# Kernel tuning notes

Measured on AMD Instinct MI355X. Metric: run time of the kernel, lower is better.

Reference implementation:

```python
import jax, jax.numpy as jnp
import numpy as np


def setup_inputs() -> dict:
    key = jax.random.key(0)
    kq, kk, kv = jax.random.split(key, 3)
    B, H, N, D = 2, 16, 2048, 128
    q = jax.random.normal(kq, (B, H, N, D), dtype=jnp.float32)
    k = jax.random.normal(kk, (B, H, N, D), dtype=jnp.float32)
    v = jax.random.normal(kv, (B, H, N, D), dtype=jnp.float32)
    return {"q": q, "k": k, "v": v, "num_sink": 4, "window_size": 1024}


def reference(q, k, v, num_sink, window_size):
    # Sink + sliding-window causal attention (single-device path of the SP wrapper).
    # Query i attends to key j iff j <= i AND (j < num_sink OR i - j < window_size).
    B, H, N, D = q.shape
    scale = 1.0 / np.sqrt(D).astype(np.float32)
    i = jnp.arange(N)[:, None]   # query positions
    j = jnp.arange(N)[None, :]   # key positions
    mask = (j <= i) & ((j < num_sink) | ((i - j) < window_size))  # [N, N]
    scores = jnp.einsum('bhid,bhjd->bhij', q, k) * scale          # [B,H,N,N]
    scores = jnp.where(mask, scores, jnp.finfo(scores.dtype).min)
    attn = jax.nn.softmax(scores, axis=-1)
    return jnp.einsum('bhij,bhjd->bhid', attn, v)
```

## Files before the change

kernel.cpp:

```cpp
#include <hip/hip_runtime.h>
#include <stdint.h>

#define NN 2048
#define DD 128
#define BHH 32
#define QT 64
#define KT 64
#define NQT (NN / QT)

typedef short v8s __attribute__((ext_vector_type(8)));
typedef short v4s __attribute__((ext_vector_type(4)));
typedef float v4f __attribute__((ext_vector_type(4)));

__device__ __forceinline__ unsigned short f2bf(float x) {
  unsigned u = __builtin_bit_cast(unsigned, x);
  u += 0x7fffu + ((u >> 16) & 1u);
  return (unsigned short)(u >> 16);
}

__device__ __forceinline__ v8s cvt8(const float* __restrict__ p) {
  v8s r;
#pragma unroll
  for (int j = 0; j < 8; j++) r[j] = (short)f2bf(p[j]);
  return r;
}

__global__ void prep(const float* __restrict__ K, const float* __restrict__ V,
                     unsigned short* __restrict__ Kb, unsigned short* __restrict__ Vt) {
  const int z = blockIdx.z;
  const int tid = threadIdx.x;
  if (z >= BHH) {
    const int bh = z - BHH;
    const int chunk = blockIdx.y * 32 + blockIdx.x;
    size_t base = (size_t)bh * NN * DD + (size_t)chunk * 4096 + (size_t)tid * 16;
#pragma unroll
    for (int h = 0; h < 2; h++)
      *(v8s*)(Kb + base + h * 8) = cvt8(K + base + h * 8);
    return;
  }
  __shared__ unsigned short t[64 * 68];
  const int bh = z;
  const int n0 = blockIdx.x * 64, d0 = blockIdx.y * 64;
  const float* src = V + ((size_t)bh * NN + n0) * DD + d0;
#pragma unroll
  for (int p = 0; p < 4; p++) {
    int r = p * 16 + (tid >> 4);
    int c = (tid & 15) * 4;
    v4f f = *(const v4f*)(src + (size_t)r * DD + c);
    v4s u;
#pragma unroll
    for (int j = 0; j < 4; j++) u[j] = (short)f2bf(f[j]);
    *(v4s*)(t + r * 68 + c) = u;
  }
  __syncthreads();
  unsigned short* dst = Vt + ((size_t)bh * DD + d0) * NN + n0;
#pragma unroll
  for (int p = 0; p < 2; p++) {
    int d = p * 32 + (tid >> 3);
    int nc = (tid & 7) * 8;
    v8s o;
#pragma unroll
    for (int j = 0; j < 8; j++) o[j] = (short)t[(nc + j) * 68 + d];
    *(v8s*)(dst + (size_t)d * NN + nc) = o;
  }
}

template <bool KBF, bool USE_VT>
__global__ __launch_bounds__(256, 4) void attn(
    const float* __restrict__ Q,
    const float* __restrict__ Kf, const unsigned short* __restrict__ Kb,
    const unsigned short* __restrict__ Vt, const float* __restrict__ Vf,
    const int* __restrict__ nsp, const int* __restrict__ wsp,
    float* __restrict__ O) {
  const int ns = nsp[0], win = wsp[0];
  const int j = blockIdx.x;
  const int bh = j & 31;
  const int jobid = j >> 5;
  int qis[2], njobs;
  if (jobid < 16) { njobs = 1; qis[0] = 31 - jobid; qis[1] = 0; }
  else { int p = jobid - 16; njobs = 2; qis[0] = 15 - p; qis[1] = p; }

  const int tid = threadIdx.x;
  const int w = tid >> 6;
  const int l = tid & 63;
  const int lo = l & 15, q4 = l >> 4;

  __shared__ __align__(16) unsigned short Kl[KT * DD];
  __shared__ __align__(16) unsigned short Vl[KT * DD];
  __shared__ __align__(16) unsigned short Pl[4 * 16 * KT];

  const float csc = 0.088388347648318447f * 1.4426950408889634f;
  unsigned short* Pw = Pl + w * 1024;
  const int rb = q4 * 4;

  for (int ji = 0; ji < njobs; ji++) {
    const int q0 = qis[ji] * QT;
    const int qrow0 = q0 + w * 16;

    v8s qf[4];
    {
      const float* qb = Q + ((size_t)bh * NN + qrow0 + lo) * DD + q4 * 8;
#pragma unroll
      for (int kc = 0; kc < 4; kc++) qf[kc] = cvt8(qb + kc * 32);
    }

    float lsum[4];
    v4f oa[8];
#pragma unroll
    for (int r = 0; r < 4; r++) lsum[r] = 0.f;
#pragma unroll
    for (int nc = 0; nc < 8; nc++) oa[nc] = (v4f){0.f, 0.f, 0.f, 0.f};

    const size_t koff0 = ((size_t)bh * NN + w * 16 + lo) * DD + q4 * 8;

    for (int kb = 0; kb < q0 + QT; kb += KT) {
      if ((kb >= ns) && (kb + KT - 1 < q0 - win + 1)) continue;

      v8s kst[4];
      {
        size_t g = koff0 + (size_t)kb * DD;
#pragma unroll
        for (int kc = 0; kc < 4; kc++)
          kst[kc] = KBF ? *(const v8s*)(Kb + g + kc * 32) : cvt8(Kf + g + kc * 32);
      }
      v8s vst[4];
      if (USE_VT) {
#pragma unroll
        for (int i = 0; i < 4; i++) {
          int f = w * 4 + i, kt = f >> 3, nc = f & 7;
          vst[i] = *(const v8s*)(Vt + ((size_t)bh * DD + nc * 16 + lo) * NN + kb +
                                 kt * 32 + q4 * 8);
        }
      }

      __syncthreads();
#pragma unroll
      for (int kc = 0; kc < 4; kc++)
        *(v8s*)(Kl + (w * 4 + kc) * 512 + l * 8) = kst[kc];
      if (USE_VT) {
#pragma unroll
        for (int i = 0; i < 4; i++)
          *(v8s*)(Vl + (w * 4 + i) * 512 + l * 8) = vst[i];
      }
      __syncthreads();

      v4f s[4];
#pragma unroll
      for (int ct = 0; ct < 4; ct++) {
        s[ct] = (v4f){0.f, 0.f, 0.f, 0.f};
#pragma unroll
        for (int kc = 0; kc < 4; kc++) {
          v8s kf = *(const v8s*)(Kl + (ct * 4 + kc) * 512 + l * 8);
          s[ct] = __builtin_amdgcn_mfma_f32_16x16x32_bf16(qf[kc], kf, s[ct], 0, 0, 0);
        }
      }
#pragma unroll
      for (int ct = 0; ct < 4; ct++) {
        int kj = kb + ct * 16 + lo;
#pragma unroll
        for (int r = 0; r < 4; r++) {
          int qi = qrow0 + rb + r;
          bool valid = (kj <= qi) && ((kj < ns) || (qi - kj < win));
          s[ct][r] = valid ? __builtin_amdgcn_exp2f(s[ct][r] * csc) : 0.f;
        }
      }
#pragma unroll
      for (int r = 0; r < 4; r++)
        lsum[r] += (s[0][r] + s[1][r]) + (s[2][r] + s[3][r]);

#pragma unroll
      for (int ct = 0; ct < 4; ct++) {
#pragma unroll
        for (int r = 0; r < 4; r++) {
          int row = rb + r;
          int idx = (ct >> 1) * 512 + (row + 16 * ((ct & 1) * 2 + ((l >> 3) & 1))) * 8 + (l & 7);
          Pw[idx] = f2bf(s[ct][r]);
        }
      }
#pragma unroll
      for (int kt = 0; kt < 2; kt++) {
        v8s pf = *(const v8s*)(Pw + kt * 512 + l * 8);
#pragma unroll
        for (int nc = 0; nc < 8; nc++) {
          v8s vf;
          if (USE_VT) {
            vf = *(const v8s*)(Vl + (kt * 8 + nc) * 512 + l * 8);
          } else {
#pragma unroll
            for (int jj = 0; jj < 8; jj++) {
              size_t vi = ((size_t)bh * NN + kb + kt * 32 + q4 * 8 + jj) * DD + nc * 16 + lo;
              vf[jj] = (short)f2bf(Vf[vi]);
            }
          }
          oa[nc] = __builtin_amdgcn_mfma_f32_16x16x32_bf16(pf, vf, oa[nc], 0, 0, 0);
        }
      }
    }

    float inv[4];
#pragma unroll
    for (int r = 0; r < 4; r++) {
      float v = lsum[r];
      v += __shfl_xor(v, 1, 64);
      v += __shfl_xor(v, 2, 64);
      v += __shfl_xor(v, 4, 64);
      v += __shfl_xor(v, 8, 64);
      inv[r] = 1.f / v;
    }
    float* ob = O + ((size_t)bh * NN + qrow0) * DD;
#pragma unroll
    for (int nc = 0; nc < 8; nc++)
#pragma unroll
      for (int r = 0; r < 4; r++)
        ob[(size_t)(rb + r) * DD + nc * 16 + lo] = oa[nc][r] * inv[r];
  }
}

extern "C" void kernel_launch(void* const* d_in, const int* in_sizes, int n_in,
                              void* d_out, int out_size, void* d_ws, size_t ws_size,
                              hipStream_t stream) {
  const float* q = (const float*)d_in[0];
  const float* k = (const float*)d_in[1];
  const float* v = (const float*)d_in[2];
  const int* nsp = (const int*)d_in[3];
  const int* wsp = (const int*)d_in[4];
  float* out = (float*)d_out;

  const size_t half = (size_t)BHH * NN * DD * sizeof(unsigned short);
  unsigned short* kbf = (unsigned short*)d_ws;
  unsigned short* vt = (unsigned short*)((char*)d_ws + half);
  const int nblocks = BHH * 24;

  if (ws_size >= 2 * half) {
    prep<<<dim3(32, 2, 2 * BHH), 256, 0, stream>>>(k, v, kbf, vt);
    attn<true, true><<<nblocks, 256, 0, stream>>>(q, k, kbf, vt, v, nsp, wsp, out);
  } else if (ws_size >= half) {
    prep<<<dim3(32, 2, BHH), 256, 0, stream>>>(k, v, nullptr, (unsigned short*)d_ws);
    attn<false, true><<<nblocks, 256, 0, stream>>>(q, k, nullptr, (unsigned short*)d_ws, v, nsp, wsp, out);
  } else {
    attn<false, false><<<nblocks, 256, 0, stream>>>(q, k, nullptr, nullptr, v, nsp, wsp, out);
  }
}
```

Measured before the change: 200.8 us.

## Load K/V fragments directly from global, skip sink-only gaps, XCD-aware block mapping

The attention kernel drops the shared-memory staging of K and V and the two barriers per tile, loading MFMA fragments straight from global or L2, with Q pre-scaled and the score MFMA operands swapped. It adds a sink-only fast path that processes just the first 16 sink keys and then starts at the window, a mask-free branch for fully valid tiles, setprio around MFMA blocks, and a block-to-bh mapping that keeps each head on one XCD. The prep kernel uses packed bf16 conversion and vectorized LDS transposes. The trade-off is more redundant global loads per wave, since each wave now loads whole K tiles itself, and lower occupancy from launch bounds 3.

After: 316.4 us. +57.5%, slower.

```diff
diff --git a/kernel.cpp b/kernel.cpp
--- a/kernel.cpp
+++ b/kernel.cpp
@@ -6,11 +6,13 @@
 #define BHH 32
 #define QT 64
 #define KT 64
-#define NQT (NN / QT)
 
 typedef short v8s __attribute__((ext_vector_type(8)));
 typedef short v4s __attribute__((ext_vector_type(4)));
 typedef float v4f __attribute__((ext_vector_type(4)));
+typedef unsigned int u32;
+typedef u32 u32x2 __attribute__((ext_vector_type(2)));
+typedef u32 u32x4 __attribute__((ext_vector_type(4)));
 
 __device__ __forceinline__ unsigned short f2bf(float x) {
   unsigned u = __builtin_bit_cast(unsigned, x);
@@ -25,7 +27,13 @@
   return r;
 }
 
-__global__ void prep(const float* __restrict__ K, const float* __restrict__ V,
+__device__ __forceinline__ u32 pk2(float a, float b) {
+  u32 r;
+  asm("v_cvt_pk_bf16_f32 %0, %1, %2" : "=v"(r) : "v"(a), "v"(b));
+  return r;
+}
+
+__global__ __launch_bounds__(256) void prep(const float* __restrict__ K, const float* __restrict__ V,
                      unsigned short* __restrict__ Kb, unsigned short* __restrict__ Vt) {
   const int z = blockIdx.z;
   const int tid = threadIdx.x;
@@ -33,24 +41,29 @@
     const int bh = z - BHH;
     const int chunk = blockIdx.y * 32 + blockIdx.x;
     size_t base = (size_t)bh * NN * DD + (size_t)chunk * 4096 + (size_t)tid * 16;
-#pragma unroll
-    for (int h = 0; h < 2; h++)
-      *(v8s*)(Kb + base + h * 8) = cvt8(K + base + h * 8);
+    v4f f0 = *(const v4f*)(K + base);
+    v4f f1 = *(const v4f*)(K + base + 4);
+    v4f f2 = *(const v4f*)(K + base + 8);
+    v4f f3 = *(const v4f*)(K + base + 12);
+    u32x4 w0 = { pk2(f0[0], f0[1]), pk2(f0[2], f0[3]), pk2(f1[0], f1[1]), pk2(f1[2], f1[3]) };
+    u32x4 w1 = { pk2(f2[0], f2[1]), pk2(f2[2], f2[3]), pk2(f3[0], f3[1]), pk2(f3[2], f3[3]) };
+    *(u32x4*)(Kb + base) = w0;
+    *(u32x4*)(Kb + base + 8) = w1;
     return;
   }
-  __shared__ unsigned short t[64 * 68];
+  __shared__ __align__(16) unsigned short t[64 * 68];
   const int bh = z;
   const int n0 = blockIdx.x * 64, d0 = blockIdx.y * 64;
-  const float* src = V + ((size_t)bh * NN + n0) * DD + d0;
-#pragma unroll
-  for (int p = 0; p < 4; p++) {
-    int r = p * 16 + (tid >> 4);
-    int c = (tid & 15) * 4;
-    v4f f = *(const v4f*)(src + (size_t)r * DD + c);
-    v4s u;
-#pragma unroll
-    for (int j = 0; j < 4; j++) u[j] = (short)f2bf(f[j]);
-    *(v4s*)(t + r * 68 + c) = u;
+  const int c16 = tid & 15, r4 = tid >> 4;
+  const float* src = V + ((size_t)bh * NN + n0 + r4 * 4) * DD + d0 + c16 * 4;
+  v4f f0 = *(const v4f*)(src);
+  v4f f1 = *(const v4f*)(src + DD);
+  v4f f2 = *(const v4f*)(src + 2 * DD);
+  v4f f3 = *(const v4f*)(src + 3 * DD);
+#pragma unroll
+  for (int j = 0; j < 4; j++) {
+    u32x2 w = { pk2(f0[j], f1[j]), pk2(f2[j], f3[j]) };
+    *(u32x2*)(t + (c16 * 4 + j) * 68 + r4 * 4) = w;
   }
   __syncthreads();
   unsigned short* dst = Vt + ((size_t)bh * DD + d0) * NN + n0;
@@ -58,24 +71,25 @@
   for (int p = 0; p < 2; p++) {
     int d = p * 32 + (tid >> 3);
     int nc = (tid & 7) * 8;
-    v8s o;
-#pragma unroll
-    for (int j = 0; j < 8; j++) o[j] = (short)t[(nc + j) * 68 + d];
+    v4s x0 = *(const v4s*)(t + d * 68 + nc);
+    v4s x1 = *(const v4s*)(t + d * 68 + nc + 4);
+    v8s o = { x0[0], x0[1], x0[2], x0[3], x1[0], x1[1], x1[2], x1[3] };
     *(v8s*)(dst + (size_t)d * NN + nc) = o;
   }
 }
 
-template <bool KBF, bool USE_VT>
-__global__ __launch_bounds__(256, 4) void attn(
+template <bool PREPPED>
+__global__ __launch_bounds__(256, 3) void attn(
     const float* __restrict__ Q,
     const float* __restrict__ Kf, const unsigned short* __restrict__ Kb,
     const unsigned short* __restrict__ Vt, const float* __restrict__ Vf,
     const int* __restrict__ nsp, const int* __restrict__ wsp,
     float* __restrict__ O) {
   const int ns = nsp[0], win = wsp[0];
-  const int j = blockIdx.x;
-  const int bh = j & 31;
-  const int jobid = j >> 5;
+  const int x = blockIdx.x;
+  const int xcd = x & 7, slot = x >> 3;
+  const int bh = xcd + 8 * (slot / 24);
+  const int jobid = slot % 24;
   int qis[2], njobs;
   if (jobid < 16) { njobs = 1; qis[0] = 31 - jobid; qis[1] = 0; }
   else { int p = jobid - 16; njobs = 2; qis[0] = 15 - p; qis[1] = p; }
@@ -85,134 +99,168 @@
   const int l = tid & 63;
   const int lo = l & 15, q4 = l >> 4;
 
-  __shared__ __align__(16) unsigned short Kl[KT * DD];
-  __shared__ __align__(16) unsigned short Vl[KT * DD];
-  __shared__ __align__(16) unsigned short Pl[4 * 16 * KT];
+  __shared__ __align__(16) unsigned short Pl[4 * 1024];
+  unsigned short* Pw = Pl + w * 1024;
+  const int prd = q4 * 128 + lo * 8;
 
   const float csc = 0.088388347648318447f * 1.4426950408889634f;
-  unsigned short* Pw = Pl + w * 1024;
-  const int rb = q4 * 4;
+
+  const unsigned short* kbase = Kb + (size_t)bh * NN * DD + (size_t)lo * DD + q4 * 8;
+  const float*         kfb   = Kf + (size_t)bh * NN * DD + (size_t)lo * DD + q4 * 8;
+  const unsigned short* vbase = Vt + (size_t)bh * DD * NN + (size_t)lo * NN + q4 * 8;
 
   for (int ji = 0; ji < njobs; ji++) {
     const int q0 = qis[ji] * QT;
     const int qrow0 = q0 + w * 16;
+    const int qi = qrow0 + lo;
 
     v8s qf[4];
     {
       const float* qb = Q + ((size_t)bh * NN + qrow0 + lo) * DD + q4 * 8;
 #pragma unroll
-      for (int kc = 0; kc < 4; kc++) qf[kc] = cvt8(qb + kc * 32);
+      for (int kc = 0; kc < 4; kc++) {
+        v8s r;
+#pragma unroll
+        for (int e = 0; e < 8; e++) r[e] = (short)f2bf(qb[kc * 32 + e] * csc);
+        qf[kc] = r;
+      }
     }
 
-    float lsum[4];
+    float lsum = 0.f;
     v4f oa[8];
 #pragma unroll
-    for (int r = 0; r < 4; r++) lsum[r] = 0.f;
-#pragma unroll
     for (int nc = 0; nc < 8; nc++) oa[nc] = (v4f){0.f, 0.f, 0.f, 0.f};
 
-    const size_t koff0 = ((size_t)bh * NN + w * 16 + lo) * DD + q4 * 8;
-
-    for (int kb = 0; kb < q0 + QT; kb += KT) {
-      if ((kb >= ns) && (kb + KT - 1 < q0 - win + 1)) continue;
-
-      v8s kst[4];
-      {
-        size_t g = koff0 + (size_t)kb * DD;
-#pragma unroll
-        for (int kc = 0; kc < 4; kc++)
-          kst[kc] = KBF ? *(const v8s*)(Kb + g + kc * 32) : cvt8(Kf + g + kc * 32);
-      }
-      v8s vst[4];
-      if (USE_VT) {
-#pragma unroll
-        for (int i = 0; i < 4; i++) {
-          int f = w * 4 + i, kt = f >> 3, nc = f & 7;
-          vst[i] = *(const v8s*)(Vt + ((size_t)bh * DD + nc * 16 + lo) * NN + kb +
-                                 kt * 32 + q4 * 8);
-        }
-      }
-
-      __syncthreads();
-#pragma unroll
-      for (int kc = 0; kc < 4; kc++)
-        *(v8s*)(Kl + (w * 4 + kc) * 512 + l * 8) = kst[kc];
-      if (USE_VT) {
-#pragma unroll
-        for (int i = 0; i < 4; i++)
-          *(v8s*)(Vl + (w * 4 + i) * 512 + l * 8) = vst[i];
-      }
-      __syncthreads();
-
+    auto tile = [&](int kb) {
+      v8s kf[4][4];
+#pragma unroll
+      for (int ct = 0; ct < 4; ct++)
+#pragma unroll
+        for (int kc = 0; kc < 4; kc++) {
+          if constexpr (PREPPED)
+            kf[ct][kc] = *(const v8s*)(kbase + (size_t)(kb + ct * 16) * DD + kc * 32);
+          else
+            kf[ct][kc] = cvt8(kfb + (size_t)(kb + ct * 16) * DD + kc * 32);
+        }
       v4f s[4];
+      __builtin_amdgcn_s_setprio(1);
 #pragma unroll
       for (int ct = 0; ct < 4; ct++) {
         s[ct] = (v4f){0.f, 0.f, 0.f, 0.f};
 #pragma unroll
-        for (int kc = 0; kc < 4; kc++) {
-          v8s kf = *(const v8s*)(Kl + (ct * 4 + kc) * 512 + l * 8);
-          s[ct] = __builtin_amdgcn_mfma_f32_16x16x32_bf16(qf[kc], kf, s[ct], 0, 0, 0);
-        }
-      }
+        for (int kc = 0; kc < 4; kc++)
+          s[ct] = __builtin_amdgcn_mfma_f32_16x16x32_bf16(kf[ct][kc], qf[kc], s[ct], 0, 0, 0);
+      }
+      __builtin_amdgcn_s_setprio(0);
+
+      const bool full = (kb + KT - 1 <= qrow0) && (kb + win >= qrow0 + 16);
+      if (full) {
+#pragma unroll
+        for (int ct = 0; ct < 4; ct++)
+#pragma unroll
+          for (int r = 0; r < 4; r++) s[ct][r] = __builtin_amdgcn_exp2f(s[ct][r]);
+      } else {
+#pragma unroll
+        for (int ct = 0; ct < 4; ct++) {
+          const int kjb = kb + ct * 16 + q4 * 4;
+#pragma unroll
+          for (int r = 0; r < 4; r++) {
+            const int kj = kjb + r;
+            const bool valid = (kj <= qi) && ((kj < ns) || (qi - kj < win));
+            s[ct][r] = valid ? __builtin_amdgcn_exp2f(s[ct][r]) : 0.f;
+          }
+        }
+      }
+#pragma unroll
+      for (int ct = 0; ct < 4; ct++)
+        lsum += (s[ct][0] + s[ct][1]) + (s[ct][2] + s[ct][3]);
+
 #pragma unroll
       for (int ct = 0; ct < 4; ct++) {
-        int kj = kb + ct * 16 + lo;
-#pragma unroll
-        for (int r = 0; r < 4; r++) {
-          int qi = qrow0 + rb + r;
-          bool valid = (kj <= qi) && ((kj < ns) || (qi - kj < win));
-          s[ct][r] = valid ? __builtin_amdgcn_exp2f(s[ct][r] * csc) : 0.f;
-        }
-      }
-#pragma unroll
-      for (int r = 0; r < 4; r++)
-        lsum[r] += (s[0][r] + s[1][r]) + (s[2][r] + s[3][r]);
-
-#pragma unroll
-      for (int ct = 0; ct < 4; ct++) {
-#pragma unroll
-        for (int r = 0; r < 4; r++) {
-          int row = rb + r;
-          int idx = (ct >> 1) * 512 + (row + 16 * ((ct & 1) * 2 + ((l >> 3) & 1))) * 8 + (l & 7);
-          Pw[idx] = f2bf(s[ct][r]);
-        }
+        u32x2 pw = { pk2(s[ct][0], s[ct][1]), pk2(s[ct][2], s[ct][3]) };
+        *(u32x2*)(Pw + (ct >> 1) * 512 + ((ct & 1) * 2 + (q4 >> 1)) * 128 + lo * 8 + (q4 & 1) * 4) = pw;
       }
 #pragma unroll
       for (int kt = 0; kt < 2; kt++) {
-        v8s pf = *(const v8s*)(Pw + kt * 512 + l * 8);
+        v8s pf = *(const v8s*)(Pw + kt * 512 + prd);
+        __builtin_amdgcn_s_setprio(1);
 #pragma unroll
         for (int nc = 0; nc < 8; nc++) {
           v8s vf;
-          if (USE_VT) {
-            vf = *(const v8s*)(Vl + (kt * 8 + nc) * 512 + l * 8);
-          } else {
-#pragma unroll
-            for (int jj = 0; jj < 8; jj++) {
-              size_t vi = ((size_t)bh * NN + kb + kt * 32 + q4 * 8 + jj) * DD + nc * 16 + lo;
-              vf[jj] = (short)f2bf(Vf[vi]);
-            }
+          if constexpr (PREPPED)
+            vf = *(const v8s*)(vbase + (size_t)(nc * 16) * NN + kb + kt * 32);
+          else {
+#pragma unroll
+            for (int e = 0; e < 8; e++)
+              vf[e] = (short)f2bf(Vf[((size_t)bh * NN + kb + kt * 32 + q4 * 8 + e) * DD + nc * 16 + lo]);
           }
           oa[nc] = __builtin_amdgcn_mfma_f32_16x16x32_bf16(pf, vf, oa[nc], 0, 0, 0);
         }
+        __builtin_amdgcn_s_setprio(0);
+      }
+    };
+
+    const int wstart = q0 - win + 1;
+    const bool sinkonly = (wstart > KT - 1) && (ns <= 16);
+    if (sinkonly) {
+      {
+        v8s kf0[4];
+#pragma unroll
+        for (int kc = 0; kc < 4; kc++) {
+          if constexpr (PREPPED) kf0[kc] = *(const v8s*)(kbase + (size_t)kc * 32);
+          else kf0[kc] = cvt8(kfb + (size_t)kc * 32);
+        }
+        v4f s0 = (v4f){0.f, 0.f, 0.f, 0.f};
+#pragma unroll
+        for (int kc = 0; kc < 4; kc++)
+          s0 = __builtin_amdgcn_mfma_f32_16x16x32_bf16(kf0[kc], qf[kc], s0, 0, 0, 0);
+#pragma unroll
+        for (int r = 0; r < 4; r++) {
+          const int kj = q4 * 4 + r;
+          const bool valid = (kj < ns) && (kj <= qi);
+          s0[r] = valid ? __builtin_amdgcn_exp2f(s0[r]) : 0.f;
+        }
+        lsum += (s0[0] + s0[1]) + (s0[2] + s0[3]);
+        u32x2 pw = { pk2(s0[0], s0[1]), pk2(s0[2], s0[3]) };
+        *(u32x2*)(Pw + (q4 >> 1) * 128 + lo * 8 + (q4 & 1) * 4) = pw;
+        u32x2 pz = { 0u, 0u };
+        *(u32x2*)(Pw + (2 + (q4 >> 1)) * 128 + lo * 8 + (q4 & 1) * 4) = pz;
+        v8s pf = *(const v8s*)(Pw + prd);
+#pragma unroll
+        for (int nc = 0; nc < 8; nc++) {
+          v8s vf;
+          if constexpr (PREPPED)
+            vf = *(const v8s*)(vbase + (size_t)(nc * 16) * NN);
+          else {
+#pragma unroll
+            for (int e = 0; e < 8; e++)
+              vf[e] = (short)f2bf(Vf[((size_t)bh * NN + q4 * 8 + e) * DD + nc * 16 + lo]);
+          }
+          oa[nc] = __builtin_amdgcn_mfma_f32_16x16x32_bf16(pf, vf, oa[nc], 0, 0, 0);
+        }
+      }
+      const int kbw = (wstart >> 6) << 6;
+      for (int kb = kbw; kb < q0 + QT; kb += KT) tile(kb);
+    } else {
+      for (int kb = 0; kb < q0 + QT; kb += KT) {
+        if ((kb >= ns) && (kb + KT - 1 < wstart)) continue;
+        tile(kb);
       }
     }
 
-    float inv[4];
-#pragma unroll
-    for (int r = 0; r < 4; r++) {
-      float v = lsum[r];
-      v += __shfl_xor(v, 1, 64);
-      v += __shfl_xor(v, 2, 64);
-      v += __shfl_xor(v, 4, 64);
-      v += __shfl_xor(v, 8, 64);
-      inv[r] = 1.f / v;
-    }
+    float lt = lsum;
+    lt += __shfl_xor(lt, 16, 64);
+    lt += __shfl_xor(lt, 32, 64);
+    const float inv = 1.f / lt;
+    float invr[4];
+#pragma unroll
+    for (int r = 0; r < 4; r++) invr[r] = __shfl(inv, (l & 48) | (q4 * 4 + r), 64);
     float* ob = O + ((size_t)bh * NN + qrow0) * DD;
 #pragma unroll
     for (int nc = 0; nc < 8; nc++)
 #pragma unroll
       for (int r = 0; r < 4; r++)
-        ob[(size_t)(rb + r) * DD + nc * 16 + lo] = oa[nc][r] * inv[r];
+        ob[(size_t)(q4 * 4 + r) * DD + nc * 16 + lo] = oa[nc][r] * invr[r];
   }
 }
 
@@ -227,17 +275,14 @@
   float* out = (float*)d_out;
 
   const size_t half = (size_t)BHH * NN * DD * sizeof(unsigned short);
-  unsigned short* kbf = (unsigned short*)d_ws;
-  unsigned short* vt = (unsigned short*)((char*)d_ws + half);
   const int nblocks = BHH * 24;
 
   if (ws_size >= 2 * half) {
+    unsigned short* kbf = (unsigned short*)d_ws;
+    unsigned short* vt = (unsigned short*)((char*)d_ws + half);
     prep<<<dim3(32, 2, 2 * BHH), 256, 0, stream>>>(k, v, kbf, vt);
-    attn<true, true><<<nblocks, 256, 0, stream>>>(q, k, kbf, vt, v, nsp, wsp, out);
-  } else if (ws_size >= half) {
-    prep<<<dim3(32, 2, BHH), 256, 0, stream>>>(k, v, nullptr, (unsigned short*)d_ws);
-    attn<false, true><<<nblocks, 256, 0, stream>>>(q, k, nullptr, (unsigned short*)d_ws, v, nsp, wsp, out);
+    attn<true><<<nblocks, 256, 0, stream>>>(q, k, kbf, vt, v, nsp, wsp, out);
   } else {
-    attn<false, false><<<nblocks, 256, 0, stream>>>(q, k, nullptr, nullptr, v, nsp, wsp, out);
-  }
-}
+    attn<false><<<nblocks, 256, 0, stream>>>(q, k, nullptr, nullptr, v, nsp, wsp, out);
+  }
+}
```
